# Kernel tuning notes

Hardware: AMD Instinct MI355X
Metric: run time of the kernel (lower is better)

Reference implementation:

```python
import jax, jax.numpy as jnp
import numpy as np

D_MODEL = 768
H = 12
D_K = D_MODEL // H


def setup_inputs() -> dict:
    key = jax.random.key(0)
    ks = jax.random.split(key, 12)
    B, S = 2, 2048
    scale = 1.0 / np.sqrt(D_MODEL)
    q = jax.random.normal(ks[0], (B, S, D_MODEL), jnp.float32)
    k = jax.random.normal(ks[1], (B, S, D_MODEL), jnp.float32)
    v = jax.random.normal(ks[2], (B, S, D_MODEL), jnp.float32)
    mask = jnp.tril(jnp.ones((S, S), jnp.int32))[None, None]  # causal [1,1,S,S]
    wq = jax.random.normal(ks[3], (D_MODEL, D_MODEL), jnp.float32) * scale
    wk = jax.random.normal(ks[4], (D_MODEL, D_MODEL), jnp.float32) * scale
    wv = jax.random.normal(ks[5], (D_MODEL, D_MODEL), jnp.float32) * scale
    wo = jax.random.normal(ks[6], (D_MODEL, D_MODEL), jnp.float32) * scale
    bq = jax.random.normal(ks[7], (D_MODEL,), jnp.float32) * 0.02
    bk = jax.random.normal(ks[8], (D_MODEL,), jnp.float32) * 0.02
    bv = jax.random.normal(ks[9], (D_MODEL,), jnp.float32) * 0.02
    bo = jax.random.normal(ks[10], (D_MODEL,), jnp.float32) * 0.02
    return {"q": q, "k": k, "v": v, "mask": mask,
            "wq": wq, "bq": bq, "wk": wk, "bk": bk,
            "wv": wv, "bv": bv, "wo": wo, "bo": bo}


def reference(q, k, v, mask, wq, bq, wk, bk, wv, bv, wo, bo):
    B, S, _ = q.shape
    # projections (torch Linear: x @ W.T + b)
    qh = (q @ wq.T + bq).reshape(B, S, H, D_K).transpose(0, 2, 1, 3)  # [B,H,S,Dk]
    kh = (k @ wk.T + bk).reshape(B, S, H, D_K).transpose(0, 2, 1, 3)
    vh = (v @ wv.T + bv).reshape(B, S, H, D_K).transpose(0, 2, 1, 3)
    scores = jnp.einsum('bhqd,bhkd->bhqk', qh, kh) / np.sqrt(D_K)
    scores = jnp.where(mask == 0, -jnp.inf, scores)
    attn = jax.nn.softmax(scores, axis=-1)  # dropout p=0.0 (eval) -> identity
    x = jnp.einsum('bhqk,bhkd->bhqd', attn, vh)
    x = x.transpose(0, 2, 1, 3).reshape(B, S, D_MODEL)
    return x @ wo.T + bo
```

## Files before the change

kernel.cpp:

```cpp
#include <hip/hip_runtime.h>
#include <hip/hip_bf16.h>

#define DM 768
#define NH 12
#define DK 64
#define SEQ 2048
#define NB 2
#define M_ (NB*SEQ)
#define XN 3145728
#define WN 589824

typedef __bf16 bf16;
typedef bf16 bf16x2 __attribute__((ext_vector_type(2)));
typedef bf16 bf16x4 __attribute__((ext_vector_type(4)));
typedef bf16 bf16x8 __attribute__((ext_vector_type(8)));
typedef float f32x4 __attribute__((ext_vector_type(4)));

__device__ __forceinline__ f32x4 mfma16(bf16x8 a, bf16x8 b, f32x4 c) {
    return __builtin_amdgcn_mfma_f32_16x16x32_bf16(a, b, c, 0, 0, 0);
}

__device__ __forceinline__ void gload_lds16(const bf16* g, bf16* l) {
    __builtin_amdgcn_global_load_lds(
        (const __attribute__((address_space(1))) void*)g,
        (__attribute__((address_space(3))) void*)l, 16, 0, 0);
}

__global__ __launch_bounds__(256) void convert_kernel(
    const float* __restrict__ q, const float* __restrict__ k, const float* __restrict__ v,
    const float* __restrict__ wq, const float* __restrict__ wk, const float* __restrict__ wv,
    const float* __restrict__ wo, bf16* __restrict__ Xb, bf16* __restrict__ Wb)
{
    long long e = ((long long)blockIdx.x * 256 + threadIdx.x) * 8;
    const float* src; bf16* dst;
    if (e < 3LL * XN) {
        int z = (int)(e / XN);
        src = (z == 0 ? q : z == 1 ? k : v) + (e - (long long)z * XN);
        dst = Xb + e;
    } else {
        long long e2 = e - 3LL * XN;
        int z = (int)(e2 / WN);
        src = (z == 0 ? wq : z == 1 ? wk : z == 2 ? wv : wo) + (e2 - (long long)z * WN);
        dst = Wb + e2;
    }
    f32x4 a = *(const f32x4*)src;
    f32x4 b = *(const f32x4*)(src + 4);
    bf16x8 o;
#pragma unroll
    for (int j = 0; j < 4; ++j) { o[j] = (bf16)a[j]; o[j + 4] = (bf16)b[j]; }
    *(bf16x8*)dst = o;
}

__global__ __launch_bounds__(256) void qkv_gemm_kernel(
    const bf16* __restrict__ Xb, const bf16* __restrict__ Wb,
    const float* __restrict__ bq, const float* __restrict__ bk, const float* __restrict__ bv,
    bf16* __restrict__ Qh, bf16* __restrict__ Kh, bf16* __restrict__ Vt)
{
    __shared__ bf16 lds[12288];
    int z = blockIdx.z;
    const bf16* Ab = Xb + (size_t)z * XN;
    const bf16* Wz = Wb + (size_t)z * WN;
    const float* Bi = (z == 0) ? bq : (z == 1) ? bk : bv;

    int t = threadIdx.x;
    int lane = t & 63, w = t >> 6;
    int g = lane >> 4, c = lane & 15;
    int wm = (w >> 1) * 64, wn = (w & 1) * 32;
    int m0 = blockIdx.x * 128, n0 = blockIdx.y * 64;

    f32x4 acc[4][2] = {};

    const bf16* Agp[4];
#pragma unroll
    for (int r = 0; r < 4; ++r) {
        int e = r * 2048 + t * 8;
        int kk = e >> 12, mm = (e & 4095) >> 5, k8 = e & 31;
        Agp[r] = Ab + (size_t)(m0 + mm) * DM + kk * 32 + k8;
    }
    const bf16* Bgp[2];
#pragma unroll
    for (int r = 0; r < 2; ++r) {
        int e = r * 2048 + t * 8;
        int kk = e >> 11, nn = (e & 2047) >> 5, k8 = e & 31;
        Bgp[r] = Wz + (size_t)(n0 + nn) * DM + kk * 32 + k8;
    }

    for (int kt = 0; kt < 12; ++kt) {
#pragma unroll
        for (int r = 0; r < 4; ++r)
            gload_lds16(Agp[r] + kt * 64, &lds[r * 2048 + t * 8]);
#pragma unroll
        for (int r = 0; r < 2; ++r)
            gload_lds16(Bgp[r] + kt * 64, &lds[8192 + r * 2048 + t * 8]);
        __syncthreads();
        bf16x8 af[4][2], bfr[2][2];
#pragma unroll
        for (int kk = 0; kk < 2; ++kk) {
#pragma unroll
            for (int mi = 0; mi < 4; ++mi)
                af[mi][kk] = *(const bf16x8*)&lds[kk * 4096 + (wm + mi * 16 + c) * 32 + g * 8];
#pragma unroll
            for (int ni = 0; ni < 2; ++ni)
                bfr[ni][kk] = *(const bf16x8*)&lds[8192 + kk * 2048 + (wn + ni * 16 + c) * 32 + g * 8];
        }
#pragma unroll
        for (int mi = 0; mi < 4; ++mi)
#pragma unroll
            for (int ni = 0; ni < 2; ++ni) {
                acc[mi][ni] = mfma16(af[mi][0], bfr[ni][0], acc[mi][ni]);
                acc[mi][ni] = mfma16(af[mi][1], bfr[ni][1], acc[mi][ni]);
            }
        __syncthreads();
    }

    int b_ = m0 >> 11, sbase = m0 & (SEQ - 1);
    int h = blockIdx.y;
    if (z == 0) {
#pragma unroll
        for (int ni = 0; ni < 2; ++ni) {
            int nl = wn + ni * 16 + c;
            float bias = Bi[n0 + nl];
#pragma unroll
            for (int mi = 0; mi < 4; ++mi)
#pragma unroll
                for (int r = 0; r < 4; ++r) {
                    int s = sbase + wm + mi * 16 + g * 4 + r;
                    Qh[((size_t)(b_ * NH + h) * SEQ + s) * DK + nl] = (bf16)(acc[mi][ni][r] + bias);
                }
        }
    } else if (z == 1) {
#pragma unroll
        for (int ni = 0; ni < 2; ++ni) {
            int nl = wn + ni * 16 + c;
            float bias = Bi[n0 + nl];
            int chunk = nl >> 3, e = nl & 7;
#pragma unroll
            for (int mi = 0; mi < 4; ++mi)
#pragma unroll
                for (int r = 0; r < 4; ++r) {
                    int s = sbase + wm + mi * 16 + g * 4 + r;
                    int pos = ((chunk ^ (s & 7)) << 3) + e;
                    Kh[((size_t)(b_ * NH + h) * SEQ + s) * DK + pos] = (bf16)(acc[mi][ni][r] + bias);
                }
        }
    } else {
#pragma unroll
        for (int ni = 0; ni < 2; ++ni) {
            int nl = wn + ni * 16 + c;
            float bias = Bi[n0 + nl];
#pragma unroll
            for (int mi = 0; mi < 4; ++mi) {
                bf16x4 pk;
#pragma unroll
                for (int r = 0; r < 4; ++r) pk[r] = (bf16)(acc[mi][ni][r] + bias);
                int sb = wm + mi * 16;
                int grp64 = sb >> 6, grp = (sb >> 5) & 1, bb = (sb >> 4) & 1;
                int chi = 4 * grp + g;
                int col = grp64 * 64 + (((chi ^ (nl & 7)) << 3)) + 4 * bb;
                *(bf16x4*)&lds[nl * 136 + col] = pk;
            }
        }
        __syncthreads();
        int dk = t >> 2, sc = (t & 3) * 32;
        bf16* vdst = Vt + ((size_t)(b_ * NH + h) * DK + dk) * SEQ + sbase + sc;
#pragma unroll
        for (int j = 0; j < 4; ++j)
            *(bf16x8*)(vdst + j * 8) = *(const bf16x8*)&lds[dk * 136 + sc + j * 8];
    }
}

__global__ __launch_bounds__(256) void o_gemm_kernel(
    const bf16* __restrict__ Xo, const bf16* __restrict__ Wo,
    const float* __restrict__ bo, float* __restrict__ out)
{
    __shared__ bf16 lds[12288];
    int t = threadIdx.x;
    int lane = t & 63, w = t >> 6;
    int g = lane >> 4, c = lane & 15;
    int wm = (w >> 1) * 64, wn = (w & 1) * 32;
    int m0 = blockIdx.x * 128, n0 = blockIdx.y * 64;

    f32x4 acc[4][2] = {};

    const bf16* Agp[4];
#pragma unroll
    for (int r = 0; r < 4; ++r) {
        int e = r * 2048 + t * 8;
        int kk = e >> 12, mm = (e & 4095) >> 5, k8 = e & 31;
        Agp[r] = Xo + (size_t)(m0 + mm) * DM + kk * 32 + k8;
    }
    const bf16* Bgp[2];
#pragma unroll
    for (int r = 0; r < 2; ++r) {
        int e = r * 2048 + t * 8;
        int kk = e >> 11, nn = (e & 2047) >> 5, k8 = e & 31;
        Bgp[r] = Wo + (size_t)(n0 + nn) * DM + kk * 32 + k8;
    }

    for (int kt = 0; kt < 12; ++kt) {
#pragma unroll
        for (int r = 0; r < 4; ++r)
            gload_lds16(Agp[r] + kt * 64, &lds[r * 2048 + t * 8]);
#pragma unroll
        for (int r = 0; r < 2; ++r)
            gload_lds16(Bgp[r] + kt * 64, &lds[8192 + r * 2048 + t * 8]);
        __syncthreads();
        bf16x8 af[4][2], bfr[2][2];
#pragma unroll
        for (int kk = 0; kk < 2; ++kk) {
#pragma unroll
            for (int mi = 0; mi < 4; ++mi)
                af[mi][kk] = *(const bf16x8*)&lds[kk * 4096 + (wm + mi * 16 + c) * 32 + g * 8];
#pragma unroll
            for (int ni = 0; ni < 2; ++ni)
                bfr[ni][kk] = *(const bf16x8*)&lds[8192 + kk * 2048 + (wn + ni * 16 + c) * 32 + g * 8];
        }
#pragma unroll
        for (int mi = 0; mi < 4; ++mi)
#pragma unroll
            for (int ni = 0; ni < 2; ++ni) {
                acc[mi][ni] = mfma16(af[mi][0], bfr[ni][0], acc[mi][ni]);
                acc[mi][ni] = mfma16(af[mi][1], bfr[ni][1], acc[mi][ni]);
            }
        __syncthreads();
    }

#pragma unroll
    for (int ni = 0; ni < 2; ++ni) {
        int n = n0 + wn + ni * 16 + c;
        float bias = bo[n];
#pragma unroll
        for (int mi = 0; mi < 4; ++mi)
#pragma unroll
            for (int r = 0; r < 4; ++r)
                out[(size_t)(m0 + wm + mi * 16 + g * 4 + r) * DM + n] = acc[mi][ni][r] + bias;
    }
}

__global__ __launch_bounds__(256) void attn_kernel(
    const bf16* __restrict__ Qh, const bf16* __restrict__ Kh, const bf16* __restrict__ Vt,
    bf16* __restrict__ Xo)
{
    __shared__ bf16 kt_lds[2][4096];
    __shared__ bf16 vt_lds[2][4096];

    int blk = blockIdx.x;
    int bh = blk % (NB * NH);
    int J  = 15 - blk / (NB * NH);
    int t = threadIdx.x;
    int w = t >> 6, lane = t & 63;
    int g = lane >> 4, c = lane & 15;
    int sw = c & 7;
    const bf16* Qb = Qh + (size_t)bh * SEQ * DK;
    const bf16* Kb = Kh + (size_t)bh * SEQ * DK;
    const bf16* Vb = Vt + (size_t)bh * DK * SEQ;
    int b_ = bh / NH, h = bh % NH;

    const float SCL = 0.125f * 1.4426950408889634f;

    int qa = J * 128 + w * 32;
    bf16x8 qaf0 = *(const bf16x8*)(Qb + (size_t)(qa + c) * DK + g * 8);
    bf16x8 qaf1 = *(const bf16x8*)(Qb + (size_t)(qa + c) * DK + 32 + g * 8);
    bf16x8 qbf0 = *(const bf16x8*)(Qb + (size_t)(qa + 16 + c) * DK + g * 8);
    bf16x8 qbf1 = *(const bf16x8*)(Qb + (size_t)(qa + 16 + c) * DK + 32 + g * 8);

    float ma = -INFINITY, la = 0.f, mb = -INFINITY, lb = 0.f;
    f32x4 oa[4] = {}, ob[4] = {};
    int nkt = 2 * J + 2;

    auto stage = [&](int kt, int buf) {
        int kb = kt * 64;
        const bf16* kg = Kb + (size_t)kb * DK + t * 8;
        gload_lds16(kg,        &kt_lds[buf][t * 8]);
        gload_lds16(kg + 2048, &kt_lds[buf][2048 + t * 8]);
        int dvr = t >> 3, colc = (t & 7) * 8;
        const bf16* vg = Vb + (size_t)dvr * SEQ + kb + colc;
        gload_lds16(vg,                  &vt_lds[buf][t * 8]);
        gload_lds16(vg + (size_t)32 * SEQ, &vt_lds[buf][2048 + t * 8]);
    };

    auto group = [&](int qbase, int kb, float& m_st, float& l_st, f32x4* o,
                     bf16x8 q0f, bf16x8 q1f, bf16x8 (&kf)[4][2], bf16x8 (&vf)[2][4]) {
        if (kb > qbase + 15) return;
        bool masked = (kb + 63 > qbase);
        int myq = qbase + c;
        float p_[4][4];
#pragma unroll
        for (int i = 0; i < 4; ++i) {
            f32x4 a = {};
            a = mfma16(kf[i][0], q0f, a);
            a = mfma16(kf[i][1], q1f, a);
            if (masked) {
#pragma unroll
                for (int r = 0; r < 4; ++r) {
                    int key = kb + i * 16 + g * 4 + r;
                    p_[i][r] = (key <= myq) ? a[r] * SCL : -INFINITY;
                }
            } else {
#pragma unroll
                for (int r = 0; r < 4; ++r) p_[i][r] = a[r] * SCL;
            }
        }
        float m0_ = fmaxf(fmaxf(p_[0][0], p_[0][1]), fmaxf(p_[0][2], p_[0][3]));
        float m1_ = fmaxf(fmaxf(p_[1][0], p_[1][1]), fmaxf(p_[1][2], p_[1][3]));
        float m2_ = fmaxf(fmaxf(p_[2][0], p_[2][1]), fmaxf(p_[2][2], p_[2][3]));
        float m3_ = fmaxf(fmaxf(p_[3][0], p_[3][1]), fmaxf(p_[3][2], p_[3][3]));
        float mx = fmaxf(fmaxf(m0_, m1_), fmaxf(m2_, m3_));
        mx = fmaxf(mx, __shfl_xor(mx, 16, 64));
        mx = fmaxf(mx, __shfl_xor(mx, 32, 64));
        float m_new = fmaxf(m_st, mx);
        float alpha = exp2f(m_st - m_new);
        m_st = m_new;
#pragma unroll
        for (int i = 0; i < 4; ++i)
#pragma unroll
            for (int r = 0; r < 4; ++r)
                p_[i][r] = exp2f(p_[i][r] - m_new);
        float s0_ = (p_[0][0] + p_[0][1]) + (p_[0][2] + p_[0][3]);
        float s1_ = (p_[1][0] + p_[1][1]) + (p_[1][2] + p_[1][3]);
        float s2_ = (p_[2][0] + p_[2][1]) + (p_[2][2] + p_[2][3]);
        float s3_ = (p_[3][0] + p_[3][1]) + (p_[3][2] + p_[3][3]);
        float psum = (s0_ + s1_) + (s2_ + s3_);
        psum += __shfl_xor(psum, 16, 64);
        psum += __shfl_xor(psum, 32, 64);
        l_st = l_st * alpha + psum;
#pragma unroll
        for (int t2 = 0; t2 < 4; ++t2)
#pragma unroll
            for (int r = 0; r < 4; ++r) o[t2][r] *= alpha;
        bf16x8 pa0, pa1;
#pragma unroll
        for (int jj = 0; jj < 8; ++jj) {
            pa0[jj] = (bf16)p_[jj >> 2][jj & 3];
            pa1[jj] = (bf16)p_[2 + (jj >> 2)][jj & 3];
        }
#pragma unroll
        for (int t2 = 0; t2 < 4; ++t2) {
            o[t2] = mfma16(vf[0][t2], pa0, o[t2]);
            o[t2] = mfma16(vf[1][t2], pa1, o[t2]);
        }
    };

    stage(0, 0);
    for (int kt = 0; kt < nkt; ++kt) {
        __syncthreads();
        if (kt + 1 < nkt) stage(kt + 1, (kt + 1) & 1);
        int kb = kt * 64;
        if (kb <= qa + 31) {
            int buf = kt & 1;
            bf16x8 kf[4][2];
#pragma unroll
            for (int i = 0; i < 4; ++i) {
                kf[i][0] = *(const bf16x8*)&kt_lds[buf][(16 * i + c) * 64 + ((g ^ sw) << 3)];
                kf[i][1] = *(const bf16x8*)&kt_lds[buf][(16 * i + c) * 64 + (((4 + g) ^ sw) << 3)];
            }
            bf16x8 vf[2][4];
#pragma unroll
            for (int grp = 0; grp < 2; ++grp)
#pragma unroll
                for (int t2 = 0; t2 < 4; ++t2)
                    vf[grp][t2] = *(const bf16x8*)&vt_lds[buf][(16 * t2 + c) * 64 + (((grp * 4 + g) ^ sw) << 3)];
            group(qa,      kb, ma, la, oa, qaf0, qaf1, kf, vf);
            group(qa + 16, kb, mb, lb, ob, qbf0, qbf1, kf, vf);
        }
    }

    float inva = 1.f / la, invb = 1.f / lb;
#pragma unroll
    for (int t2 = 0; t2 < 4; ++t2) {
        bf16x4 sa, sb2;
#pragma unroll
        for (int r = 0; r < 4; ++r) {
            sa[r]  = (bf16)(oa[t2][r] * inva);
            sb2[r] = (bf16)(ob[t2][r] * invb);
        }
        *(bf16x4*)&Xo[(size_t)(b_ * SEQ + qa + c) * DM + h * DK + t2 * 16 + g * 4] = sa;
        *(bf16x4*)&Xo[(size_t)(b_ * SEQ + qa + 16 + c) * DM + h * DK + t2 * 16 + g * 4] = sb2;
    }
}

extern "C" void kernel_launch(void* const* d_in, const int* in_sizes, int n_in,
                              void* d_out, int out_size, void* d_ws, size_t ws_size,
                              hipStream_t stream) {
    const float* q  = (const float*)d_in[0];
    const float* k  = (const float*)d_in[1];
    const float* v  = (const float*)d_in[2];
    const float* wq = (const float*)d_in[4];
    const float* bq = (const float*)d_in[5];
    const float* wk = (const float*)d_in[6];
    const float* bk = (const float*)d_in[7];
    const float* wv = (const float*)d_in[8];
    const float* bv = (const float*)d_in[9];
    const float* wo = (const float*)d_in[10];
    const float* bo = (const float*)d_in[11];

    bf16* Xb = (bf16*)d_ws;
    bf16* Wb = Xb + 3 * (size_t)XN;
    bf16* Qh = Wb + 4 * (size_t)WN;
    bf16* Kh = Qh + (size_t)XN;
    bf16* Vt = Kh + (size_t)XN;
    bf16* Xo = Xb;
    float* out = (float*)d_out;

    dim3 blk(256);
    convert_kernel<<<dim3(5760), blk, 0, stream>>>(q, k, v, wq, wk, wv, wo, Xb, Wb);
    qkv_gemm_kernel<<<dim3(M_ / 128, DM / 64, 3), blk, 0, stream>>>(
        Xb, Wb, bq, bk, bv, Qh, Kh, Vt);
    attn_kernel<<<dim3(24 * 16), blk, 0, stream>>>(Qh, Kh, Vt, Xo);
    o_gemm_kernel<<<dim3(M_ / 128, DM / 64), blk, 0, stream>>>(Xo, Wb + 3 * (size_t)WN, bo, out);
}
```

Baseline: 227.4 us.

## Shrink attention blocks to 32 queries with 128 threads for finer causal work split

The attention kernel now launches 1536 blocks of 128 threads, each covering 32 query rows (16 per wave), instead of 384 blocks of 256 threads covering 128 rows each. Each wave now tracks one 16-row query group rather than two, and the per-block key-tile count follows the smaller causal extent, so blocks do less wasted work near the diagonal and the grid balances better across CUs. In exchange, each K/V tile is loaded from global memory by more blocks, which raises memory and L2 traffic and lowers MFMA reuse per staged tile.

```diff
diff --git a/kernel.cpp b/kernel.cpp
--- a/kernel.cpp
+++ b/kernel.cpp
@@ -156,7 +156,7 @@
                 int sb = wm + mi * 16;
                 int grp64 = sb >> 6, grp = (sb >> 5) & 1, bb = (sb >> 4) & 1;
                 int chi = 4 * grp + g;
-                int col = grp64 * 64 + (((chi ^ (nl & 7)) << 3)) + 4 * bb;
+                int col = grp64 * 64 + ((chi ^ (nl & 7)) << 3) + 4 * bb;
                 *(bf16x4*)&lds[nl * 136 + col] = pk;
             }
         }
@@ -237,7 +237,7 @@
     }
 }
 
-__global__ __launch_bounds__(256) void attn_kernel(
+__global__ __launch_bounds__(128) void attn_kernel(
     const bf16* __restrict__ Qh, const bf16* __restrict__ Kh, const bf16* __restrict__ Vt,
     bf16* __restrict__ Xo)
 {
@@ -246,7 +246,7 @@
 
     int blk = blockIdx.x;
     int bh = blk % (NB * NH);
-    int J  = 15 - blk / (NB * NH);
+    int J  = 63 - blk / (NB * NH);
     int t = threadIdx.x;
     int w = t >> 6, lane = t & 63;
     int g = lane >> 4, c = lane & 15;
@@ -258,38 +258,54 @@
 
     const float SCL = 0.125f * 1.4426950408889634f;
 
-    int qa = J * 128 + w * 32;
-    bf16x8 qaf0 = *(const bf16x8*)(Qb + (size_t)(qa + c) * DK + g * 8);
-    bf16x8 qaf1 = *(const bf16x8*)(Qb + (size_t)(qa + c) * DK + 32 + g * 8);
-    bf16x8 qbf0 = *(const bf16x8*)(Qb + (size_t)(qa + 16 + c) * DK + g * 8);
-    bf16x8 qbf1 = *(const bf16x8*)(Qb + (size_t)(qa + 16 + c) * DK + 32 + g * 8);
-
-    float ma = -INFINITY, la = 0.f, mb = -INFINITY, lb = 0.f;
-    f32x4 oa[4] = {}, ob[4] = {};
-    int nkt = 2 * J + 2;
+    int qa = J * 32 + w * 16;
+    bf16x8 qf0 = *(const bf16x8*)(Qb + (size_t)(qa + c) * DK + g * 8);
+    bf16x8 qf1 = *(const bf16x8*)(Qb + (size_t)(qa + c) * DK + 32 + g * 8);
+
+    float m_st = -INFINITY, l_st = 0.f;
+    f32x4 o[4] = {};
+    int myq = qa + c;
+    int nkt = (J >> 1) + 1;
 
     auto stage = [&](int kt, int buf) {
         int kb = kt * 64;
         const bf16* kg = Kb + (size_t)kb * DK + t * 8;
-        gload_lds16(kg,        &kt_lds[buf][t * 8]);
-        gload_lds16(kg + 2048, &kt_lds[buf][2048 + t * 8]);
+#pragma unroll
+        for (int i = 0; i < 4; ++i)
+            gload_lds16(kg + i * 1024, &kt_lds[buf][i * 1024 + t * 8]);
         int dvr = t >> 3, colc = (t & 7) * 8;
         const bf16* vg = Vb + (size_t)dvr * SEQ + kb + colc;
-        gload_lds16(vg,                  &vt_lds[buf][t * 8]);
-        gload_lds16(vg + (size_t)32 * SEQ, &vt_lds[buf][2048 + t * 8]);
+#pragma unroll
+        for (int i = 0; i < 4; ++i)
+            gload_lds16(vg + (size_t)(16 * i) * SEQ, &vt_lds[buf][i * 1024 + t * 8]);
     };
 
-    auto group = [&](int qbase, int kb, float& m_st, float& l_st, f32x4* o,
-                     bf16x8 q0f, bf16x8 q1f, bf16x8 (&kf)[4][2], bf16x8 (&vf)[2][4]) {
-        if (kb > qbase + 15) return;
-        bool masked = (kb + 63 > qbase);
-        int myq = qbase + c;
+    stage(0, 0);
+    for (int kt = 0; kt < nkt; ++kt) {
+        __syncthreads();
+        if (kt + 1 < nkt) stage(kt + 1, (kt + 1) & 1);
+        int kb = kt * 64;
+        int buf = kt & 1;
+        bf16x8 kf[4][2];
+#pragma unroll
+        for (int i = 0; i < 4; ++i) {
+            kf[i][0] = *(const bf16x8*)&kt_lds[buf][(16 * i + c) * 64 + ((g ^ sw) << 3)];
+            kf[i][1] = *(const bf16x8*)&kt_lds[buf][(16 * i + c) * 64 + (((4 + g) ^ sw) << 3)];
+        }
+        bf16x8 vf[2][4];
+#pragma unroll
+        for (int grp = 0; grp < 2; ++grp)
+#pragma unroll
+            for (int t2 = 0; t2 < 4; ++t2)
+                vf[grp][t2] = *(const bf16x8*)&vt_lds[buf][(16 * t2 + c) * 64 + (((grp * 4 + g) ^ sw) << 3)];
+
+        bool masked = (kb + 63 > qa);
         float p_[4][4];
 #pragma unroll
         for (int i = 0; i < 4; ++i) {
             f32x4 a = {};
-            a = mfma16(kf[i][0], q0f, a);
-            a = mfma16(kf[i][1], q1f, a);
+            a = mfma16(kf[i][0], qf0, a);
+            a = mfma16(kf[i][1], qf1, a);
             if (masked) {
 #pragma unroll
                 for (int r = 0; r < 4; ++r) {
@@ -339,43 +355,15 @@
             o[t2] = mfma16(vf[0][t2], pa0, o[t2]);
             o[t2] = mfma16(vf[1][t2], pa1, o[t2]);
         }
-    };
-
-    stage(0, 0);
-    for (int kt = 0; kt < nkt; ++kt) {
-        __syncthreads();
-        if (kt + 1 < nkt) stage(kt + 1, (kt + 1) & 1);
-        int kb = kt * 64;
-        if (kb <= qa + 31) {
-            int buf = kt & 1;
-            bf16x8 kf[4][2];
-#pragma unroll
-            for (int i = 0; i < 4; ++i) {
-                kf[i][0] = *(const bf16x8*)&kt_lds[buf][(16 * i + c) * 64 + ((g ^ sw) << 3)];
-                kf[i][1] = *(const bf16x8*)&kt_lds[buf][(16 * i + c) * 64 + (((4 + g) ^ sw) << 3)];
-            }
-            bf16x8 vf[2][4];
-#pragma unroll
-            for (int grp = 0; grp < 2; ++grp)
-#pragma unroll
-                for (int t2 = 0; t2 < 4; ++t2)
-                    vf[grp][t2] = *(const bf16x8*)&vt_lds[buf][(16 * t2 + c) * 64 + (((grp * 4 + g) ^ sw) << 3)];
-            group(qa,      kb, ma, la, oa, qaf0, qaf1, kf, vf);
-            group(qa + 16, kb, mb, lb, ob, qbf0, qbf1, kf, vf);
-        }
-    }
-
-    float inva = 1.f / la, invb = 1.f / lb;
+    }
+
+    float inv = 1.f / l_st;
 #pragma unroll
     for (int t2 = 0; t2 < 4; ++t2) {
-        bf16x4 sa, sb2;
-#pragma unroll
-        for (int r = 0; r < 4; ++r) {
-            sa[r]  = (bf16)(oa[t2][r] * inva);
-            sb2[r] = (bf16)(ob[t2][r] * invb);
-        }
+        bf16x4 sa;
+#pragma unroll
+        for (int r = 0; r < 4; ++r) sa[r] = (bf16)(o[t2][r] * inv);
         *(bf16x4*)&Xo[(size_t)(b_ * SEQ + qa + c) * DM + h * DK + t2 * 16 + g * 4] = sa;
-        *(bf16x4*)&Xo[(size_t)(b_ * SEQ + qa + 16 + c) * DM + h * DK + t2 * 16 + g * 4] = sb2;
     }
 }
 
@@ -406,6 +394,6 @@
     convert_kernel<<<dim3(5760), blk, 0, stream>>>(q, k, v, wq, wk, wv, wo, Xb, Wb);
     qkv_gemm_kernel<<<dim3(M_ / 128, DM / 64, 3), blk, 0, stream>>>(
         Xb, Wb, bq, bk, bv, Qh, Kh, Vt);
-    attn_kernel<<<dim3(24 * 16), blk, 0, stream>>>(Qh, Kh, Vt, Xo);
+    attn_kernel<<<dim3(24 * 64), dim3(128), 0, stream>>>(Qh, Kh, Vt, Xo);
     o_gemm_kernel<<<dim3(M_ / 128, DM / 64), blk, 0, stream>>>(Xo, Wb + 3 * (size_t)WN, bo, out);
 }
```

After: 205.0 us. 1.11x faster.
